# Kernel optimization log

Measured on AMD Instinct MI355X. Metric: run time of the kernel, lower is better.

Reference implementation:

```python
import jax, jax.numpy as jnp
import numpy as np

N = 49998      # num nodes, divisible by (neg_sample_ratio + 2) = 3
E = 800000     # num edges (avg degree 16)
DIM_IN = 128
DIM_OUT = 32
H0 = 8         # heads layer 0
H1 = 1         # heads layer 1


def setup_inputs() -> dict:
    key = jax.random.key(0)
    ks = jax.random.split(key, 16)
    s = 0.05
    x = jax.random.normal(ks[0], (N, DIM_IN), dtype=jnp.float32)
    src = jax.random.randint(ks[1], (E,), 0, N)
    dst = jax.random.randint(ks[2], (E,), 0, N)
    W0 = jax.random.normal(ks[3], (DIM_IN, H0 * DIM_OUT), dtype=jnp.float32) * s
    al0 = jax.random.normal(ks[4], (H0, DIM_OUT), dtype=jnp.float32) * s
    ar0 = jax.random.normal(ks[5], (H0, DIM_OUT), dtype=jnp.float32) * s
    b0 = jnp.zeros((H0 * DIM_OUT,), dtype=jnp.float32)
    W1 = jax.random.normal(ks[6], (H0 * DIM_OUT, H1 * DIM_OUT), dtype=jnp.float32) * s
    al1 = jax.random.normal(ks[7], (H1, DIM_OUT), dtype=jnp.float32) * s
    ar1 = jax.random.normal(ks[8], (H1, DIM_OUT), dtype=jnp.float32) * s
    b1 = jnp.zeros((H1 * DIM_OUT,), dtype=jnp.float32)
    P1 = jax.random.normal(ks[9], (DIM_OUT, DIM_OUT), dtype=jnp.float32) * s
    pb1 = jnp.zeros((DIM_OUT,), dtype=jnp.float32)
    P2 = jax.random.normal(ks[10], (DIM_OUT, DIM_OUT), dtype=jnp.float32) * s
    pb2 = jnp.zeros((DIM_OUT,), dtype=jnp.float32)
    P3 = jax.random.normal(ks[11], (DIM_OUT, 1), dtype=jnp.float32) * s
    pb3 = jnp.zeros((1,), dtype=jnp.float32)
    return dict(x=x, src=src, dst=dst, neg_sample_ratio=1,
                W0=W0, al0=al0, ar0=ar0, b0=b0,
                W1=W1, al1=al1, ar1=ar1, b1=b1,
                P1=P1, pb1=pb1, P2=P2, pb2=pb2, P3=P3, pb3=pb3)


def gat_conv(x, src, dst, W, al, ar, b):
    """DGL GATConv: linear proj -> edge LeakyReLU score -> per-dst segment softmax -> weighted scatter-sum + bias."""
    n = x.shape[0]
    H, D = al.shape
    f = (x @ W).reshape(n, H, D)                     # [N,H,D]
    el = jnp.sum(f * al, axis=-1)                    # [N,H]
    er = jnp.sum(f * ar, axis=-1)                    # [N,H]
    e = jax.nn.leaky_relu(el[src] + er[dst], 0.2)    # [E,H] edge scores
    m = jax.ops.segment_max(e, dst, num_segments=n)  # [N,H] stable softmax max
    a = jnp.exp(e - m[dst])                          # [E,H]
    denom = jax.ops.segment_sum(a, dst, num_segments=n)  # [N,H]
    a = a / denom[dst]                               # normalized attention
    out = jax.ops.segment_sum(a[:, :, None] * f[src], dst, num_segments=n)  # [N,H,D]
    return out + b.reshape(1, H, D)


def reference(x, src, dst, neg_sample_ratio,
              W0, al0, ar0, b0, W1, al1, ar1, b1,
              P1, pb1, P2, pb2, P3, pb3):
    # layer 0: GATConv with ELU activation, flatten heads
    h = jax.nn.elu(gat_conv(x, src, dst, W0, al0, ar0, b0)).reshape(x.shape[0], -1)
    # layer 1: GATConv, no activation, mean over heads
    h = gat_conv(h, src, dst, W1, al1, ar1, b1).mean(axis=1)  # [N, DIM_OUT]

    num_edge = h.shape[0] // (neg_sample_ratio + 2)
    src_h = h[:num_edge]
    pos_dst_h = h[num_edge:2 * num_edge]
    neg_dst_h = h[2 * num_edge:]

    def predictor(z):
        z = jax.nn.relu(z @ P1 + pb1)
        z = jax.nn.relu(z @ P2 + pb2)
        return z @ P3 + pb3

    h_pos = predictor(src_h * pos_dst_h)
    h_neg = predictor(jnp.tile(src_h, (neg_sample_ratio, 1)) * neg_dst_h)
    return (h_pos, h_neg)
```

## Files before the change

kernel.cpp:

```cpp
#include <hip/hip_runtime.h>
#include <hip/hip_fp16.h>
#include <cmath>

#define CAPB 64
#define CAPF 88
#define CAP1 96
#define WA   92
#define G0_ROWS 64
#define G0_PAD 68

typedef _Float16 h2v __attribute__((ext_vector_type(2)));

__device__ __forceinline__ float dot2a(unsigned f, unsigned w, float acc) {
  return __builtin_amdgcn_fdot2(__builtin_bit_cast(h2v, f),
                                __builtin_bit_cast(h2v, w), acc, false);
}
__device__ __forceinline__ unsigned pkh2(float lo, float hi) {
  return (unsigned)__half_as_ushort(__float2half_rn(lo)) |
         ((unsigned)__half_as_ushort(__float2half_rn(hi)) << 16);
}

__global__ void k_prep(const float* __restrict__ W0, const float* __restrict__ W1,
                       unsigned* __restrict__ W0h, unsigned* __restrict__ W1ct) {
  int idx = blockIdx.x * 256 + threadIdx.x;
  if (idx < 16384) {
    int k2 = idx >> 8, c = idx & 255;
    W0h[idx] = pkh2(W0[(size_t)(2 * k2) * 256 + c], W0[(size_t)(2 * k2 + 1) * 256 + c]);
  } else if (idx < 20480) {
    int j = idx - 16384;
    int c = j >> 7, k2 = j & 127;
    W1ct[j] = pkh2(W1[(size_t)(2 * k2) * 32 + c], W1[(size_t)(2 * k2 + 1) * 32 + c]);
  }
}

__global__ void k_gemm0_scatter(const float* __restrict__ x, const unsigned* __restrict__ W0h,
                                const float* __restrict__ al, const float* __restrict__ ar,
                                const int* __restrict__ dst, const int* __restrict__ src,
                                unsigned short* __restrict__ f0h, float* __restrict__ el,
                                float* __restrict__ er, int* __restrict__ cnt,
                                int* __restrict__ ovf_cnt, int* __restrict__ bpad,
                                int* __restrict__ ovf, int N, int E, int ngemm) {
  __shared__ unsigned s_x2[64 * G0_PAD];
  int t = threadIdx.x;

  if (blockIdx.x >= ngemm) {
    int nscat = gridDim.x - ngemm;
    for (int e = (blockIdx.x - ngemm) * blockDim.x + t; e < E; e += nscat * blockDim.x) {
      int d = dst[e];
      int pos = atomicAdd(&cnt[d], 1);
      if (pos < CAPB) bpad[(size_t)d * CAPB + pos] = src[e];
      else { int op = atomicAdd(ovf_cnt, 1); ovf[op] = e; }
    }
    return;
  }

  int w = t >> 6, l = t & 63;
  int row0 = blockIdx.x * G0_ROWS;
  {
    int row = row0 + l; if (row >= N) row = N - 1;
    const float* xp = x + (size_t)row * 128 + w * 32;
#pragma unroll
    for (int j = 0; j < 8; ++j) {
      float4 v = *(const float4*)(xp + 4 * j);
      int k2 = w * 16 + 2 * j;
      s_x2[k2 * G0_PAD + l] = pkh2(v.x, v.y);
      s_x2[(k2 + 1) * G0_PAD + l] = pkh2(v.z, v.w);
    }
  }
  __syncthreads();

  float4 acc[16];
#pragma unroll
  for (int r = 0; r < 16; ++r) acc[r] = make_float4(0.f, 0.f, 0.f, 0.f);

  const unsigned* wp = W0h + 4 * l;
  int rbase = w * 16;
  for (int k2 = 0; k2 < 64; ++k2) {
    uint4 w4 = *(const uint4*)(wp + (size_t)k2 * 256);
    const unsigned* xk = &s_x2[k2 * G0_PAD + rbase];
    unsigned xv[16];
    *(uint4*)&xv[0]  = *(const uint4*)(xk);
    *(uint4*)&xv[4]  = *(const uint4*)(xk + 4);
    *(uint4*)&xv[8]  = *(const uint4*)(xk + 8);
    *(uint4*)&xv[12] = *(const uint4*)(xk + 12);
#pragma unroll
    for (int r = 0; r < 16; ++r) {
      acc[r].x = dot2a(xv[r], w4.x, acc[r].x);
      acc[r].y = dot2a(xv[r], w4.y, acc[r].y);
      acc[r].z = dot2a(xv[r], w4.z, acc[r].z);
      acc[r].w = dot2a(xv[r], w4.w, acc[r].w);
    }
  }

  int hh = l >> 3;
  float4 al4 = *(const float4*)(al + 4 * l);
  float4 ar4 = *(const float4*)(ar + 4 * l);
#pragma unroll
  for (int r = 0; r < 16; ++r) {
    int row = row0 + rbase + r;
    float4 f = acc[r];
    if (row < N) {
      ushort4 h4;
      h4.x = __half_as_ushort(__float2half_rn(f.x));
      h4.y = __half_as_ushort(__float2half_rn(f.y));
      h4.z = __half_as_ushort(__float2half_rn(f.z));
      h4.w = __half_as_ushort(__float2half_rn(f.w));
      *(ushort4*)(f0h + (size_t)row * 256 + 4 * l) = h4;
    }
    float pl = fmaf(f.x, al4.x, fmaf(f.y, al4.y, fmaf(f.z, al4.z, f.w * al4.w)));
    float pr = fmaf(f.x, ar4.x, fmaf(f.y, ar4.y, fmaf(f.z, ar4.z, f.w * ar4.w)));
#pragma unroll
    for (int off = 4; off >= 1; off >>= 1) {
      pl += __shfl_xor(pl, off, 64);
      pr += __shfl_xor(pr, off, 64);
    }
    if ((l & 7) == 0 && row < N) {
      el[row * 8 + hh] = pl;
      er[row * 8 + hh] = pr;
    }
  }
}

__global__ void k_fused0(const float* __restrict__ el, const float* __restrict__ er,
                         const unsigned short* __restrict__ f0h, const int* __restrict__ cnt,
                         const int* __restrict__ ovf_cnt, const int* __restrict__ bpad,
                         const int* __restrict__ ovf, const int* __restrict__ dstp,
                         const int* __restrict__ src, const float* __restrict__ b0,
                         const unsigned* __restrict__ W1ct, const float* __restrict__ al1,
                         const float* __restrict__ ar1, unsigned short* __restrict__ f1h,
                         float* __restrict__ el1, float* __restrict__ er1, int N) {
  __shared__ unsigned s_w1[32 * 132];
  __shared__ unsigned short s_wa[4][8 * WA];
  __shared__ int s_s[4][CAPF];
  __shared__ unsigned s_h2[4][128];

  const int t = threadIdx.x;
  for (int base = t * 4; base < 4096; base += 1024) {
    uint4 v = *(const uint4*)&W1ct[base];
    int c = base >> 7, k2 = base & 127;
    *(uint4*)&s_w1[c * 132 + k2] = v;
  }
  __syncthreads();

  const int w = __builtin_amdgcn_readfirstlane(t >> 6);
  const int l = t & 63;
  const int n = blockIdx.x * 4 + w;
  if (n >= N) return;

  int* sS = s_s[w];
  unsigned short* sWA = s_wa[w];

  const int sub = l & 31, half = l >> 5, hh = sub >> 2;
  float4 b0a = ((const float4*)(b0 + 8 * sub))[0];
  float4 b0b = ((const float4*)(b0 + 8 * sub))[1];
  float al1c = al1[sub], ar1c = ar1[sub];

  int cn = cnt[n];
  int degb = cn < CAPB ? cn : CAPB;
  if (l < degb) sS[l] = bpad[(size_t)n * CAPB + l];
  int deg = degb;
  int ovl = ovf_cnt[0];
  if (ovl) {
    int d = degb;
    if (l == 0) {
      for (int j = 0; j < ovl && d < 84; ++j) {
        int e = ovf[j];
        if (dstp[e] == n) sS[d++] = src[e];
      }
    }
    deg = __shfl(d, 0, 64);
  }

  float er_h = er[n * 8 + (l & 7)];
  float psum = 0.f;
  for (int e = l >> 3; e < deg; e += 8) {
    int sidx = sS[e];
    float v = el[sidx * 8 + (l & 7)] + er_h;
    v = v >= 0.f ? v : 0.2f * v;
    float a = __expf(v);
    sWA[(l & 7) * WA + e] = __half_as_ushort(__float2half_rn(a));
    psum += a;
  }
  psum += __shfl_xor(psum, 8, 64);
  psum += __shfl_xor(psum, 16, 64);
  psum += __shfl_xor(psum, 32, 64);
  float rs = psum > 0.f ? __builtin_amdgcn_rcpf(psum) : 0.f;

  int degp = (deg + 3) & ~3;
  if (l < degp - deg) sS[deg + l] = sS[0];
  { int pe = deg + (l >> 3); if (pe < degp) sWA[(l & 7) * WA + pe] = 0; }

  float a0 = 0.f, a1 = 0.f, a2 = 0.f, a3 = 0.f, a4 = 0.f, a5 = 0.f, a6 = 0.f, a7 = 0.f;
  if (degp > 0) {
    int2 sp = *(const int2*)&sS[2 * half];
    uint4 A = ((const uint4*)(f0h + (size_t)sp.x * 256))[sub];
    uint4 B = ((const uint4*)(f0h + (size_t)sp.y * 256))[sub];
    for (int i = 0;;) {
      int in = i + 4;
      uint4 A2, B2;
      if (in < degp) {
        int2 s2 = *(const int2*)&sS[in + 2 * half];
        A2 = ((const uint4*)(f0h + (size_t)s2.x * 256))[sub];
        B2 = ((const uint4*)(f0h + (size_t)s2.y * 256))[sub];
      }
      unsigned wp = *(const unsigned*)&sWA[hh * WA + i + 2 * half];
      unsigned lo, hi;
      lo = __builtin_amdgcn_perm(A.x, B.x, 0x01000504u);
      hi = __builtin_amdgcn_perm(A.x, B.x, 0x03020706u);
      a0 = dot2a(lo, wp, a0); a1 = dot2a(hi, wp, a1);
      lo = __builtin_amdgcn_perm(A.y, B.y, 0x01000504u);
      hi = __builtin_amdgcn_perm(A.y, B.y, 0x03020706u);
      a2 = dot2a(lo, wp, a2); a3 = dot2a(hi, wp, a3);
      lo = __builtin_amdgcn_perm(A.z, B.z, 0x01000504u);
      hi = __builtin_amdgcn_perm(A.z, B.z, 0x03020706u);
      a4 = dot2a(lo, wp, a4); a5 = dot2a(hi, wp, a5);
      lo = __builtin_amdgcn_perm(A.w, B.w, 0x01000504u);
      hi = __builtin_amdgcn_perm(A.w, B.w, 0x03020706u);
      a6 = dot2a(lo, wp, a6); a7 = dot2a(hi, wp, a7);
      if (in >= degp) break;
      i = in; A = A2; B = B2;
    }
  }
  a0 += __shfl_xor(a0, 32, 64); a1 += __shfl_xor(a1, 32, 64);
  a2 += __shfl_xor(a2, 32, 64); a3 += __shfl_xor(a3, 32, 64);
  a4 += __shfl_xor(a4, 32, 64); a5 += __shfl_xor(a5, 32, 64);
  a6 += __shfl_xor(a6, 32, 64); a7 += __shfl_xor(a7, 32, 64);

  float sc = __shfl(rs, hh, 64);
  float o0 = fmaf(a0, sc, b0a.x), o1 = fmaf(a1, sc, b0a.y);
  float o2 = fmaf(a2, sc, b0a.z), o3 = fmaf(a3, sc, b0a.w);
  float o4 = fmaf(a4, sc, b0b.x), o5 = fmaf(a5, sc, b0b.y);
  float o6 = fmaf(a6, sc, b0b.z), o7 = fmaf(a7, sc, b0b.w);
  o0 = o0 > 0.f ? o0 : expm1f(o0);  o1 = o1 > 0.f ? o1 : expm1f(o1);
  o2 = o2 > 0.f ? o2 : expm1f(o2);  o3 = o3 > 0.f ? o3 : expm1f(o3);
  o4 = o4 > 0.f ? o4 : expm1f(o4);  o5 = o5 > 0.f ? o5 : expm1f(o5);
  o6 = o6 > 0.f ? o6 : expm1f(o6);  o7 = o7 > 0.f ? o7 : expm1f(o7);
  if (half == 0) {
    uint4 hp;
    hp.x = pkh2(o0, o1); hp.y = pkh2(o2, o3);
    hp.z = pkh2(o4, o5); hp.w = pkh2(o6, o7);
    *(uint4*)&s_h2[w][4 * sub] = hp;
  }
  asm volatile("s_waitcnt lgkmcnt(0)" ::: "memory");

  const unsigned* wrow = &s_w1[sub * 132 + half * 64];
  const unsigned* hrow = &s_h2[w][half * 64];
  float p = 0.f;
#pragma unroll
  for (int j = 0; j < 64; j += 4) {
    uint4 wv = *(const uint4*)&wrow[j];
    uint4 hv = *(const uint4*)&hrow[j];
    p = dot2a(hv.x, wv.x, p);
    p = dot2a(hv.y, wv.y, p);
    p = dot2a(hv.z, wv.z, p);
    p = dot2a(hv.w, wv.w, p);
  }
  p += __shfl_xor(p, 32, 64);
  float pn = __shfl_xor(p, 1, 64);
  float pl = p * al1c, pr = p * ar1c;
#pragma unroll
  for (int off = 16; off >= 1; off >>= 1) {
    pl += __shfl_xor(pl, off, 64);
    pr += __shfl_xor(pr, off, 64);
  }
  if (half == 0 && (sub & 1) == 0)
    *(unsigned*)(f1h + (size_t)n * 32 + sub) = pkh2(p, pn);
  if (l == 0) { el1[n] = pl; er1[n] = pr; }
}

__global__ void k_fused1(const float* __restrict__ el, const float* __restrict__ er,
                         const unsigned short* __restrict__ f1h, const int* __restrict__ cnt,
                         const int* __restrict__ ovf_cnt, const int* __restrict__ bpad,
                         const int* __restrict__ ovf, const int* __restrict__ dstp,
                         const int* __restrict__ src, const float* __restrict__ b1,
                         float* __restrict__ h1, int N) {
  __shared__ int s_s[4][CAP1];
  __shared__ unsigned s_wp[4][CAP1 / 2];

  const int t = threadIdx.x;
  const int g = __builtin_amdgcn_readfirstlane(t >> 6);
  const int lane = t & 63;
  int n = blockIdx.x * 4 + g;
  int nn = n < N ? n : N - 1;
  int* sS = s_s[g];
  unsigned* sWP = s_wp[g];

  int cn = cnt[nn];
  int degb = cn < CAPB ? cn : CAPB;
  if (lane < degb) sS[lane] = bpad[(size_t)nn * CAPB + lane];
  int deg = degb;
  int ovl = ovf_cnt[0];
  if (ovl) {
    int d = degb;
    if (lane == 0) {
      for (int j = 0; j < ovl && d < CAP1 - 16; ++j) {
        int e = ovf[j];
        if (dstp[e] == nn) sS[d++] = src[e];
      }
    }
    deg = __shfl(d, 0, 64);
  }
  float er_n = er[nn];
  int degp = (deg + 15) & ~15;
  asm volatile("s_waitcnt lgkmcnt(0)" ::: "memory");
  if (deg + lane < degp) sS[deg + lane] = sS[0];

  float psum = 0.f;
  for (int i0 = 0; i0 < degp; i0 += 64) {
    int i = i0 + lane;
    float a = 0.f;
    if (i < deg) {
      float v = el[sS[i]] + er_n;
      v = v >= 0.f ? v : 0.2f * v;
      a = __expf(v);
      psum += a;
    }
    float an = __shfl_xor(a, 8, 64);
    if ((lane & 15) < 8 && i < degp)
      sWP[(i0 >> 1) + ((lane >> 4) << 3) + (lane & 7)] = pkh2(a, an);
  }
#pragma unroll
  for (int off = 32; off >= 1; off >>= 1) psum += __shfl_xor(psum, off, 64);
  float rs = psum > 0.f ? __builtin_amdgcn_rcpf(psum) : 0.f;

  asm volatile("s_waitcnt lgkmcnt(0)" ::: "memory");
  const int es = lane >> 3, q = lane & 7;
  float c0 = 0.f, c1 = 0.f, c2 = 0.f, c3 = 0.f;
  for (int i0 = 0; i0 < degp; i0 += 16) {
    int sA = sS[i0 + es], sB = sS[i0 + es + 8];
    uint2 A = *(const uint2*)(f1h + (size_t)sA * 32 + 4 * q);
    uint2 B = *(const uint2*)(f1h + (size_t)sB * 32 + 4 * q);
    unsigned wp = sWP[(i0 >> 1) + es];
    unsigned lo = __builtin_amdgcn_perm(A.x, B.x, 0x01000504u);
    unsigned hi = __builtin_amdgcn_perm(A.x, B.x, 0x03020706u);
    c0 = dot2a(lo, wp, c0); c1 = dot2a(hi, wp, c1);
    lo = __builtin_amdgcn_perm(A.y, B.y, 0x01000504u);
    hi = __builtin_amdgcn_perm(A.y, B.y, 0x03020706u);
    c2 = dot2a(lo, wp, c2); c3 = dot2a(hi, wp, c3);
  }
#pragma unroll
  for (int off = 8; off <= 32; off <<= 1) {
    c0 += __shfl_xor(c0, off, 64); c1 += __shfl_xor(c1, off, 64);
    c2 += __shfl_xor(c2, off, 64); c3 += __shfl_xor(c3, off, 64);
  }
  if (es == 0 && n < N) {
    float4 b = *(const float4*)(b1 + 4 * q);
    float4 o;
    o.x = fmaf(c0, rs, b.x); o.y = fmaf(c1, rs, b.y);
    o.z = fmaf(c2, rs, b.z); o.w = fmaf(c3, rs, b.w);
    ((float4*)(h1 + (size_t)n * 32))[q] = o;
  }
}

__global__ void k_pred(const float* __restrict__ h1, const float* __restrict__ P1,
                       const float* __restrict__ pb1, const float* __restrict__ P2,
                       const float* __restrict__ pb2, const float* __restrict__ P3,
                       const float* __restrict__ pb3, float* __restrict__ out,
                       int num_edge, int total) {
  int t = threadIdx.x;
  int lane = t & 31, grp = t >> 5;
  int k = blockIdx.x * 8 + grp;
  int kk = k < total ? k : 0;
  float z;
  if (kk < num_edge) {
    z = h1[(size_t)kk * 32 + lane] * h1[(size_t)(kk + num_edge) * 32 + lane];
  } else {
    int i = kk - num_edge;
    z = h1[(size_t)(i % num_edge) * 32 + lane] * h1[(size_t)(2 * num_edge + i) * 32 + lane];
  }
  double a1 = 0;
#pragma unroll
  for (int d = 0; d < 32; ++d)
    a1 += (double)__shfl(z, d, 32) * (double)P1[d * 32 + lane];
  float t1 = (float)(a1 + (double)pb1[lane]);
  t1 = t1 > 0.f ? t1 : 0.f;
  double a2 = 0;
#pragma unroll
  for (int d = 0; d < 32; ++d)
    a2 += (double)__shfl(t1, d, 32) * (double)P2[d * 32 + lane];
  float t2 = (float)(a2 + (double)pb2[lane]);
  t2 = t2 > 0.f ? t2 : 0.f;
  double a3 = (double)t2 * (double)P3[lane];
#pragma unroll
  for (int off = 16; off >= 1; off >>= 1) a3 += __shfl_xor(a3, off, 64);
  if (lane == 0 && k < total) out[k] = (float)(a3 + (double)pb3[0]);
}

extern "C" void kernel_launch(void* const* d_in, const int* in_sizes, int n_in,
                              void* d_out, int out_size, void* d_ws, size_t ws_size,
                              hipStream_t stream) {
  const float* x   = (const float*)d_in[0];
  const int*   src = (const int*)d_in[1];
  const int*   dst = (const int*)d_in[2];
  const float* W0  = (const float*)d_in[4];
  const float* al0 = (const float*)d_in[5];
  const float* ar0 = (const float*)d_in[6];
  const float* b0  = (const float*)d_in[7];
  const float* W1  = (const float*)d_in[8];
  const float* al1 = (const float*)d_in[9];
  const float* ar1 = (const float*)d_in[10];
  const float* b1  = (const float*)d_in[11];
  const float* P1  = (const float*)d_in[12];
  const float* pb1 = (const float*)d_in[13];
  const float* P2  = (const float*)d_in[14];
  const float* pb2 = (const float*)d_in[15];
  const float* P3  = (const float*)d_in[16];
  const float* pb3 = (const float*)d_in[17];

  int N = in_sizes[0] / 128;
  int E = in_sizes[1];
  int num_edge = N - out_size;

  size_t off = 0;
  auto alloc = [&](size_t bytes) -> void* {
    void* p = (char*)d_ws + off;
    off += (bytes + 255) & ~(size_t)255;
    return p;
  };
  unsigned short* f0h = (unsigned short*)alloc((size_t)N * 256 * 2);
  unsigned short* f1h = (unsigned short*)alloc((size_t)N * 32 * 2);
  float* h1   = (float*)alloc((size_t)N * 32 * 4);
  float* el   = (float*)alloc((size_t)N * 8 * 4);
  float* er   = (float*)alloc((size_t)N * 8 * 4);
  float* el1  = (float*)alloc((size_t)N * 4);
  float* er1  = (float*)alloc((size_t)N * 4);
  int*   cnt  = (int*)alloc((size_t)(N + 1) * 4);
  int*   bpad = (int*)alloc((size_t)N * CAPB * 4);
  int*   ovf  = (int*)alloc((size_t)E * 4);
  unsigned* W1ct = (unsigned*)alloc(4096 * 4);
  unsigned* W0h  = (unsigned*)alloc(16384 * 4);
  if (off > ws_size) return;
  int* ovf_cnt = cnt + N;

  int ngemm = (N + G0_ROWS - 1) / G0_ROWS;
  hipMemsetAsync(cnt, 0, (size_t)(N + 1) * 4, stream);
  k_prep<<<80, 256, 0, stream>>>(W0, W1, W0h, W1ct);
  k_gemm0_scatter<<<1792, 256, 0, stream>>>(x, W0h, al0, ar0, dst, src,
                                            f0h, el, er, cnt, ovf_cnt, bpad, ovf,
                                            N, E, ngemm);
  k_fused0<<<(N + 3) / 4, 256, 0, stream>>>(el, er, f0h, cnt, ovf_cnt, bpad, ovf, dst,
                                            src, b0, W1ct, al1, ar1, f1h, el1, er1, N);
  k_fused1<<<(N + 3) / 4, 256, 0, stream>>>(el1, er1, f1h, cnt, ovf_cnt, bpad, ovf, dst,
                                            src, b1, h1, N);
  k_pred<<<(out_size + 7) / 8, 256, 0, stream>>>(h1, P1, pb1, P2, pb2, P3, pb3,
                                                 (float*)d_out, num_edge, out_size);
}
```

Measured before the change: 297.2 us.

## Fold count memset into prep, widen fused0 blocks, prefetch neighbor features early

The zeroing of the count buffer moves from a separate memset into the prep kernel. The fused layer-0 kernel now uses 512-thread blocks with 8 nodes each, so the shared W1 load is amortized over more warps. Both fused kernels issue the first neighbor feature loads before the softmax score computation so the gather latency overlaps with the exp work. Layer-1 aggregation also gains a software-pipelined double-buffered loop, and an explicit LDS waitcnt is removed. The risks are higher register pressure and more shared memory per block, which can lower occupancy.

New measurement: 277.6 us. 1.07x faster.

```diff
diff --git a/kernel.cpp b/kernel.cpp
--- a/kernel.cpp
+++ b/kernel.cpp
@@ -21,13 +21,16 @@
 }
 
 __global__ void k_prep(const float* __restrict__ W0, const float* __restrict__ W1,
-                       unsigned* __restrict__ W0h, unsigned* __restrict__ W1ct) {
-  int idx = blockIdx.x * 256 + threadIdx.x;
-  if (idx < 16384) {
-    int k2 = idx >> 8, c = idx & 255;
-    W0h[idx] = pkh2(W0[(size_t)(2 * k2) * 256 + c], W0[(size_t)(2 * k2 + 1) * 256 + c]);
-  } else if (idx < 20480) {
-    int j = idx - 16384;
+                       unsigned* __restrict__ W0h, unsigned* __restrict__ W1ct,
+                       int* __restrict__ cnt, int Np1) {
+  int gid = blockIdx.x * 256 + threadIdx.x;
+  int stride = gridDim.x * 256;
+  for (int i = gid; i < Np1; i += stride) cnt[i] = 0;
+  if (gid < 16384) {
+    int k2 = gid >> 8, c = gid & 255;
+    W0h[gid] = pkh2(W0[(size_t)(2 * k2) * 256 + c], W0[(size_t)(2 * k2 + 1) * 256 + c]);
+  } else if (gid < 20480) {
+    int j = gid - 16384;
     int c = j >> 7, k2 = j & 127;
     W1ct[j] = pkh2(W1[(size_t)(2 * k2) * 32 + c], W1[(size_t)(2 * k2 + 1) * 32 + c]);
   }
@@ -130,12 +133,12 @@
                          const float* __restrict__ ar1, unsigned short* __restrict__ f1h,
                          float* __restrict__ el1, float* __restrict__ er1, int N) {
   __shared__ unsigned s_w1[32 * 132];
-  __shared__ unsigned short s_wa[4][8 * WA];
-  __shared__ int s_s[4][CAPF];
-  __shared__ unsigned s_h2[4][128];
+  __shared__ unsigned short s_wa[8][8 * WA];
+  __shared__ int s_s[8][CAPF];
+  __shared__ unsigned s_h2[8][128];
 
   const int t = threadIdx.x;
-  for (int base = t * 4; base < 4096; base += 1024) {
+  for (int base = t * 4; base < 4096; base += 2048) {
     uint4 v = *(const uint4*)&W1ct[base];
     int c = base >> 7, k2 = base & 127;
     *(uint4*)&s_w1[c * 132 + k2] = v;
@@ -144,7 +147,7 @@
 
   const int w = __builtin_amdgcn_readfirstlane(t >> 6);
   const int l = t & 63;
-  const int n = blockIdx.x * 4 + w;
+  const int n = blockIdx.x * 8 + w;
   if (n >= N) return;
 
   int* sS = s_s[w];
@@ -171,6 +174,17 @@
     deg = __shfl(d, 0, 64);
   }
 
+  int degp = (deg + 3) & ~3;
+  if (l < degp - deg) sS[deg + l] = sS[0];
+
+  uint4 A, B;
+  int2 sp;
+  if (degp > 0) {
+    sp = *(const int2*)&sS[2 * half];
+    A = ((const uint4*)(f0h + (size_t)sp.x * 256))[sub];
+    B = ((const uint4*)(f0h + (size_t)sp.y * 256))[sub];
+  }
+
   float er_h = er[n * 8 + (l & 7)];
   float psum = 0.f;
   for (int e = l >> 3; e < deg; e += 8) {
@@ -186,15 +200,10 @@
   psum += __shfl_xor(psum, 32, 64);
   float rs = psum > 0.f ? __builtin_amdgcn_rcpf(psum) : 0.f;
 
-  int degp = (deg + 3) & ~3;
-  if (l < degp - deg) sS[deg + l] = sS[0];
   { int pe = deg + (l >> 3); if (pe < degp) sWA[(l & 7) * WA + pe] = 0; }
 
   float a0 = 0.f, a1 = 0.f, a2 = 0.f, a3 = 0.f, a4 = 0.f, a5 = 0.f, a6 = 0.f, a7 = 0.f;
   if (degp > 0) {
-    int2 sp = *(const int2*)&sS[2 * half];
-    uint4 A = ((const uint4*)(f0h + (size_t)sp.x * 256))[sub];
-    uint4 B = ((const uint4*)(f0h + (size_t)sp.y * 256))[sub];
     for (int i = 0;;) {
       int in = i + 4;
       uint4 A2, B2;
@@ -300,11 +309,17 @@
     }
     deg = __shfl(d, 0, 64);
   }
+  int degp = (deg + 15) & ~15;
+  if (deg + lane < degp) sS[deg + lane] = sS[0];
+
+  const int es = lane >> 3, q = lane & 7;
+  uint2 A, B;
+  if (degp > 0) {
+    A = *(const uint2*)(f1h + (size_t)sS[es] * 32 + 4 * q);
+    B = *(const uint2*)(f1h + (size_t)sS[es + 8] * 32 + 4 * q);
+  }
+
   float er_n = er[nn];
-  int degp = (deg + 15) & ~15;
-  asm volatile("s_waitcnt lgkmcnt(0)" ::: "memory");
-  if (deg + lane < degp) sS[deg + lane] = sS[0];
-
   float psum = 0.f;
   for (int i0 = 0; i0 < degp; i0 += 64) {
     int i = i0 + lane;
@@ -323,20 +338,25 @@
   for (int off = 32; off >= 1; off >>= 1) psum += __shfl_xor(psum, off, 64);
   float rs = psum > 0.f ? __builtin_amdgcn_rcpf(psum) : 0.f;
 
-  asm volatile("s_waitcnt lgkmcnt(0)" ::: "memory");
-  const int es = lane >> 3, q = lane & 7;
   float c0 = 0.f, c1 = 0.f, c2 = 0.f, c3 = 0.f;
-  for (int i0 = 0; i0 < degp; i0 += 16) {
-    int sA = sS[i0 + es], sB = sS[i0 + es + 8];
-    uint2 A = *(const uint2*)(f1h + (size_t)sA * 32 + 4 * q);
-    uint2 B = *(const uint2*)(f1h + (size_t)sB * 32 + 4 * q);
-    unsigned wp = sWP[(i0 >> 1) + es];
-    unsigned lo = __builtin_amdgcn_perm(A.x, B.x, 0x01000504u);
-    unsigned hi = __builtin_amdgcn_perm(A.x, B.x, 0x03020706u);
-    c0 = dot2a(lo, wp, c0); c1 = dot2a(hi, wp, c1);
-    lo = __builtin_amdgcn_perm(A.y, B.y, 0x01000504u);
-    hi = __builtin_amdgcn_perm(A.y, B.y, 0x03020706u);
-    c2 = dot2a(lo, wp, c2); c3 = dot2a(hi, wp, c3);
+  if (degp > 0) {
+    for (int i0 = 0;;) {
+      int in = i0 + 16;
+      uint2 A2, B2;
+      if (in < degp) {
+        A2 = *(const uint2*)(f1h + (size_t)sS[in + es] * 32 + 4 * q);
+        B2 = *(const uint2*)(f1h + (size_t)sS[in + es + 8] * 32 + 4 * q);
+      }
+      unsigned wp = sWP[(i0 >> 1) + es];
+      unsigned lo = __builtin_amdgcn_perm(A.x, B.x, 0x01000504u);
+      unsigned hi = __builtin_amdgcn_perm(A.x, B.x, 0x03020706u);
+      c0 = dot2a(lo, wp, c0); c1 = dot2a(hi, wp, c1);
+      lo = __builtin_amdgcn_perm(A.y, B.y, 0x01000504u);
+      hi = __builtin_amdgcn_perm(A.y, B.y, 0x03020706u);
+      c2 = dot2a(lo, wp, c2); c3 = dot2a(hi, wp, c3);
+      if (in >= degp) break;
+      i0 = in; A = A2; B = B2;
+    }
   }
 #pragma unroll
   for (int off = 8; off <= 32; off <<= 1) {
@@ -433,12 +453,11 @@
   int* ovf_cnt = cnt + N;
 
   int ngemm = (N + G0_ROWS - 1) / G0_ROWS;
-  hipMemsetAsync(cnt, 0, (size_t)(N + 1) * 4, stream);
-  k_prep<<<80, 256, 0, stream>>>(W0, W1, W0h, W1ct);
+  k_prep<<<128, 256, 0, stream>>>(W0, W1, W0h, W1ct, cnt, N + 1);
   k_gemm0_scatter<<<1792, 256, 0, stream>>>(x, W0h, al0, ar0, dst, src,
                                             f0h, el, er, cnt, ovf_cnt, bpad, ovf,
                                             N, E, ngemm);
-  k_fused0<<<(N + 3) / 4, 256, 0, stream>>>(el, er, f0h, cnt, ovf_cnt, bpad, ovf, dst,
+  k_fused0<<<(N + 7) / 8, 512, 0, stream>>>(el, er, f0h, cnt, ovf_cnt, bpad, ovf, dst,
                                             src, b0, W1ct, al1, ar1, f1h, el1, er1, N);
   k_fused1<<<(N + 3) / 4, 256, 0, stream>>>(el1, er1, f1h, cnt, ovf_cnt, bpad, ovf, dst,
                                             src, b1, h1, N);
```
